# Optimization experiments

Measured on AMD Instinct MI355X. Metric: run time of the kernel, lower is better.

Reference implementation:

```python
import jax, jax.numpy as jnp
import numpy as np
from jax import lax

NSTEPS = 7
BN_EPS = 1e-5


def setup_inputs() -> dict:
    key = jax.random.key(0)
    ks = jax.random.split(key, 7)
    bs, in_ch, h, w, k = 8, 16, 256, 256, 3
    f = jax.random.normal(ks[0], (bs, in_ch, h, w), dtype=jnp.float32)
    vec_w = jax.random.normal(ks[1], (2 * in_ch, in_ch, k, k), dtype=jnp.float32) * 0.1
    vec_b = jax.random.normal(ks[2], (2 * in_ch,), dtype=jnp.float32) * 0.1
    bn_gamma = jnp.ones((2 * in_ch,), dtype=jnp.float32)
    bn_beta = jnp.zeros((2 * in_ch,), dtype=jnp.float32)
    fuse_w = jax.random.normal(ks[3], (in_ch, in_ch, NSTEPS, 1, 1), dtype=jnp.float32) * 0.1
    fuse_b = jax.random.normal(ks[4], (in_ch,), dtype=jnp.float32) * 0.1
    return {"f": f, "vec_w": vec_w, "vec_b": vec_b, "bn_gamma": bn_gamma,
            "bn_beta": bn_beta, "fuse_w": fuse_w, "fuse_b": fuse_b}


def _bilinear_sample(src, py, px):
    """Bilinear sample with zero padding (torch grid_sample align_corners=True).
    src: [N,C,H,W]; py,px: [N,H,W] pixel coordinates (row, col)."""
    N, C, H, W = src.shape
    y0 = jnp.floor(py); x0 = jnp.floor(px)
    wy1 = py - y0; wy0 = 1.0 - wy1
    wx1 = px - x0; wx0 = 1.0 - wx1
    src_flat = src.reshape(N, C, H * W)

    def gather(yi, xi):
        valid = (yi >= 0) & (yi <= H - 1) & (xi >= 0) & (xi <= W - 1)
        yc = jnp.clip(yi, 0, H - 1).astype(jnp.int32)
        xc = jnp.clip(xi, 0, W - 1).astype(jnp.int32)
        idx = (yc * W + xc).reshape(N, 1, H * W)
        vals = jnp.take_along_axis(src_flat, idx, axis=2).reshape(N, C, H, W)
        return vals * valid.astype(src.dtype)[:, None, :, :]

    out = (wy0 * wx0)[:, None] * gather(y0, x0) \
        + (wy0 * wx1)[:, None] * gather(y0, x0 + 1) \
        + (wy1 * wx0)[:, None] * gather(y0 + 1, x0) \
        + (wy1 * wx1)[:, None] * gather(y0 + 1, x0 + 1)
    return out


def _warp(src, flow, grid_y, grid_x):
    # grid + flow in pixel space; original normalizes to [-1,1] then grid_sample
    # un-normalizes with align_corners=True, which is exactly pixel coords grid+flow.
    py = grid_y[None] + flow[:, 0]
    px = grid_x[None] + flow[:, 1]
    return _bilinear_sample(src, py, px)


def reference(f, vec_w, vec_b, bn_gamma, bn_beta, fuse_w, fuse_b):
    bs, in_ch, h, w = f.shape
    # vec_conv + BatchNorm2d (training-mode batch stats, biased variance)
    vec = lax.conv_general_dilated(f, vec_w, (1, 1), [(1, 1), (1, 1)],
                                   dimension_numbers=("NCHW", "OIHW", "NCHW"))
    vec = vec + vec_b[None, :, None, None]
    mean = vec.mean(axis=(0, 2, 3))
    var = vec.var(axis=(0, 2, 3))
    vec = bn_gamma[None, :, None, None] * (vec - mean[None, :, None, None]) \
        * lax.rsqrt(var + BN_EPS)[None, :, None, None] + bn_beta[None, :, None, None]

    c = vec.shape[1]  # = 2*in_ch
    vec = vec.reshape(bs * c // 2, 2, h, w)  # per-channel 2D flow fields

    grid_y, grid_x = jnp.meshgrid(jnp.arange(h, dtype=f.dtype),
                                  jnp.arange(w, dtype=f.dtype), indexing="ij")

    # VecInt: scaling and squaring, keeping every intermediate deformation
    vec = vec * (1.0 / 2 ** NSTEPS)
    deforms = []
    for _ in range(NSTEPS):
        vec = vec + _warp(vec, vec, grid_y, grid_x)
        deforms.append(vec)

    fsrc = f.reshape(bs * in_ch, 1, h, w)
    maps = [_warp(fsrc, d, grid_y, grid_x).reshape(bs, in_ch, h, w) for d in deforms]
    stacked = jnp.stack(maps, axis=2)  # [bs, in_ch, nsteps, h, w]

    # Conv3d with kernel (nsteps,1,1) then squeeze -> per-pixel channel/step mix
    out = jnp.einsum("ocs,bcshw->bohw", fuse_w[:, :, :, 0, 0], stacked)
    out = out + fuse_b[None, :, None, None]
    return out
```

## Files before the change

### kernel.cpp

```cpp
#include <hip/hip_runtime.h>
#include <hip/hip_fp16.h>

#define H 256
#define W 256
#define BS 8
#define IC 16
#define OCH 32
#define NSTEPS 7
#define PLANE (H*W)
#define NFIELDS (BS*IC)
#define BN_N (BS*PLANE)
#define BN_EPS 1e-5f
#define PW 260
#define PSZ (260 * 260)

__global__ void transpose_w_kernel(const float* __restrict__ w,
                                   __half2* __restrict__ wTh) {
    for (int idx = threadIdx.x; idx < IC * 9 * 16; idx += blockDim.x) {
        int rc = idx >> 4;
        int p  = idx & 15;
        float lo = w[(2 * p) * (IC * 9) + rc];
        float hi = w[(2 * p + 1) * (IC * 9) + rc];
        wTh[idx] = __floats2half2_rn(lo, hi);
    }
}

__global__ void guard_zero_kernel(unsigned* __restrict__ bufA,
                                  unsigned* __restrict__ bufB,
                                  unsigned short* __restrict__ f16p) {
    int p = blockIdx.x;
    size_t pb = (size_t)p * PSZ;
    for (int i = threadIdx.x; i < 2064; i += blockDim.x) {
        int row, col;
        if (i < 1040) {
            int r = i / 260;
            row = (r == 0) ? 0 : 256 + r;
            col = i - r * 260;
        } else {
            int j = i - 1040;
            int c = j / 256;
            col = (c == 0) ? 0 : 256 + c;
            row = 1 + (j - c * 256);
        }
        size_t off = pb + (size_t)row * PW + col;
        bufA[off] = 0u;
        bufB[off] = 0u;
        f16p[off] = 0;
    }
}

__global__ __launch_bounds__(256, 4) void conv_kernel(
    const float* __restrict__ f, const __half2* __restrict__ wTh,
    const float* __restrict__ vec_b, __half2* __restrict__ vec_out,
    __half* __restrict__ f16p) {
    __shared__ __align__(16) __half sf[16][18][40];

    int blk = blockIdx.x;
    int xcd = blk & 7;
    int i   = blk >> 3;
    int b   = i >> 4;
    int j   = i & 15;
    int ty0 = ((xcd << 1) | (j >> 3)) * 16;
    int tx0 = (j & 7) * 32;
    int tid = threadIdx.x;
    int tyl = tid >> 5, txl = tid & 31;
    int y0p = ty0 + tyl, y1p = ty0 + tyl + 8, x = tx0 + txl;

    {
        int sic = tid >> 4;
        int st  = tid & 15;
        if (st < 10) {
            int gx0 = tx0 - 4 + 4 * st;
            const float* fpl = f + (size_t)(b * IC + sic) * PLANE;
            size_t fb16 = (size_t)(b * IC + sic) * PSZ;
            bool full = (gx0 >= 0) && (gx0 + 3 < W);
            bool own  = (st >= 1) && (st <= 8);
#pragma unroll
            for (int r = 0; r < 18; ++r) {
                int gy = ty0 - 1 + r;
                float4 v = make_float4(0.f, 0.f, 0.f, 0.f);
                if ((unsigned)gy < (unsigned)H) {
                    if (full) {
                        v = *(const float4*)(fpl + (size_t)gy * W + gx0);
                    } else {
                        if ((unsigned)(gx0 + 0) < (unsigned)W) v.x = fpl[(size_t)gy * W + gx0 + 0];
                        if ((unsigned)(gx0 + 1) < (unsigned)W) v.y = fpl[(size_t)gy * W + gx0 + 1];
                        if ((unsigned)(gx0 + 2) < (unsigned)W) v.z = fpl[(size_t)gy * W + gx0 + 2];
                        if ((unsigned)(gx0 + 3) < (unsigned)W) v.w = fpl[(size_t)gy * W + gx0 + 3];
                    }
                }
                __half2 h01 = __floats2half2_rn(v.x, v.y);
                __half2 h23 = __floats2half2_rn(v.z, v.w);
                union { __half2 h[2]; float2 f2; } u;
                u.h[0] = h01; u.h[1] = h23;
                *(float2*)&sf[sic][r][4 * st] = u.f2;
                if (own && r >= 1 && r <= 16) {
                    __half* fp = f16p + fb16 + (size_t)(gy + 1) * PW + (gx0 + 1);
                    fp[0] = __low2half(h01);
                    fp[1] = __high2half(h01);
                    fp[2] = __low2half(h23);
                    fp[3] = __high2half(h23);
                }
            }
        }
    }

    __half2 acc0[16], acc1[16];
#pragma unroll
    for (int p = 0; p < 16; ++p) {
        __half2 bp = __floats2half2_rn(vec_b[2 * p], vec_b[2 * p + 1]);
        acc0[p] = bp; acc1[p] = bp;
    }

    __syncthreads();

#pragma unroll 2
    for (int ic = 0; ic < 16; ++ic) {
#pragma unroll
        for (int k = 0; k < 9; ++k) {
            int ky = k / 3, kx = k - ky * 3;
            __half2 fv0 = __half2half2(sf[ic][tyl + ky][txl + kx + 3]);
            __half2 fv1 = __half2half2(sf[ic][tyl + 8 + ky][txl + kx + 3]);
            const __half2* wrow = wTh + (ic * 9 + k) * 16;
#pragma unroll
            for (int p = 0; p < 16; ++p) {
                __half2 wv = wrow[p];
                acc0[p] = __hfma2(fv0, wv, acc0[p]);
                acc1[p] = __hfma2(fv1, wv, acc1[p]);
            }
        }
    }

#pragma unroll
    for (int c = 0; c < IC; ++c) {
        size_t pb = (size_t)(b * IC + c) * PLANE;
        vec_out[pb + y0p * W + x] = acc0[c];
        vec_out[pb + y1p * W + x] = acc1[c];
    }
}

__global__ __launch_bounds__(256) void stats_kernel(
    const __half2* __restrict__ vec, float* __restrict__ stats) {
    int blk   = blockIdx.x;
    int n     = blk >> 4;
    int chunk = blk & 15;
    const float4* p4 = (const float4*)(vec + (size_t)n * PLANE + chunk * 4096);
    int tid = threadIdx.x;

    float s0 = 0.f, s1 = 0.f, q0 = 0.f, q1 = 0.f;
#pragma unroll 2
    for (int i = tid; i < 1024; i += 256) {
        float4 w = p4[i];
        const __half2* hh = (const __half2*)&w;
#pragma unroll
        for (int q = 0; q < 4; ++q) {
            float2 v = __half22float2(hh[q]);
            s0 += v.x; s1 += v.y;
            q0 = fmaf(v.x, v.x, q0);
            q1 = fmaf(v.y, v.y, q1);
        }
    }
#pragma unroll
    for (int off = 32; off > 0; off >>= 1) {
        s0 += __shfl_down(s0, off, 64);
        s1 += __shfl_down(s1, off, 64);
        q0 += __shfl_down(q0, off, 64);
        q1 += __shfl_down(q1, off, 64);
    }
    __shared__ float red[4][4];
    int wave = tid >> 6, lane = tid & 63;
    if (lane == 0) {
        red[wave][0] = s0; red[wave][1] = s1;
        red[wave][2] = q0; red[wave][3] = q1;
    }
    __syncthreads();
    if (tid == 0) {
        float t0 = 0.f, t1 = 0.f, t2 = 0.f, t3 = 0.f;
#pragma unroll
        for (int wv = 0; wv < 4; ++wv) {
            t0 += red[wv][0]; t1 += red[wv][1];
            t2 += red[wv][2]; t3 += red[wv][3];
        }
        int ch0 = 2 * (n & 15);
        atomicAdd(stats + ch0,          t0);
        atomicAdd(stats + ch0 + 1,      t1);
        atomicAdd(stats + 32 + ch0,     t2);
        atomicAdd(stats + 32 + ch0 + 1, t3);
    }
}

__global__ void finalize_kernel(const float* __restrict__ stats,
                                const float* __restrict__ gamma,
                                const float* __restrict__ beta,
                                float* __restrict__ AB) {
    int ch = threadIdx.x;
    if (ch < 2 * IC) {
        const float invN = 1.f / (float)BN_N;
        float mean = stats[ch] * invN;
        float var  = stats[32 + ch] * invN - mean * mean;
        float rs   = rsqrtf(var + BN_EPS);
        float a    = gamma[ch] * rs;
        AB[ch]      = a * (1.f / 128.f);
        AB[32 + ch] = (beta[ch] - a * mean) * (1.f / 128.f);
    }
}

__device__ __forceinline__ void tap_setup(float py, float px,
                                          int* o, float* wt) {
    float ffy = floorf(py), ffx = floorf(px);
    int y0 = (int)ffy, x0 = (int)ffx;
    float wy1 = py - ffy, wy0 = 1.f - wy1;
    float wx1 = px - ffx, wx0 = 1.f - wx1;
    bool vy0 = (unsigned)y0 < (unsigned)H, vy1 = (unsigned)(y0 + 1) < (unsigned)H;
    bool vx0 = (unsigned)x0 < (unsigned)W, vx1 = (unsigned)(x0 + 1) < (unsigned)W;
    int yc0 = min(max(y0, 0), H - 1), yc1 = min(max(y0 + 1, 0), H - 1);
    int xc0 = min(max(x0, 0), W - 1), xc1 = min(max(x0 + 1, 0), W - 1);
    o[0] = yc0 * W + xc0; o[1] = yc0 * W + xc1;
    o[2] = yc1 * W + xc0; o[3] = yc1 * W + xc1;
    wt[0] = (vy0 && vx0) ? wy0 * wx0 : 0.f;
    wt[1] = (vy0 && vx1) ? wy0 * wx1 : 0.f;
    wt[2] = (vy1 && vx0) ? wy1 * wx0 : 0.f;
    wt[3] = (vy1 && vx1) ? wy1 * wx1 : 0.f;
}

__device__ __forceinline__ void tap_fast(float py, float px,
                                         int& o, float* wt) {
    float pyc = fminf(fmaxf(py, -1.f), 256.f);
    float pxc = fminf(fmaxf(px, -1.f), 256.f);
    float fy = floorf(pyc), fx = floorf(pxc);
    int y0 = (int)fy, x0 = (int)fx;
    float wy1 = pyc - fy, wy0 = 1.f - wy1;
    float wx1 = pxc - fx, wx0 = 1.f - wx1;
    o = (y0 + 1) * PW + (x0 + 1);
    wt[0] = wy0 * wx0; wt[1] = wy0 * wx1;
    wt[2] = wy1 * wx0; wt[3] = wy1 * wx1;
}

template <bool FIRST, bool LAST>
__global__ __launch_bounds__(256) void step_kernel(
    const __half2* __restrict__ vinRaw, const __half2* __restrict__ vinPad,
    __half2* __restrict__ voutPad, const __half* __restrict__ f16p,
    const float* __restrict__ AB, const float* __restrict__ fw,
    const float* __restrict__ fb, __half* __restrict__ accp,
    float* __restrict__ out, int step) {
    int blk = blockIdx.x;
    int xcd = blk & 7;
    int i   = blk >> 3;
    int b   = i >> 5;
    int h   = (xcd << 5) | (i & 31);
    int tx  = threadIdx.x;
    int idx_raw = h * W + tx;
    int idx_pad = (h + 1) * PW + tx + 1;
    const size_t baseR = (size_t)b * IC * PLANE;
    const size_t baseP = (size_t)b * IC * PSZ;

    float mv[IC];

#pragma unroll 2
    for (int g = 0; g < 4; ++g) {
        float a0j[4], b0j[4], a1j[4], b1j[4];
        float fy[4], fx[4];
        float wt[4][4];
        int   ob[4];
        int   om[4][4];
        const __half2* pl[4];
        float2 vc[4];

#pragma unroll
        for (int j = 0; j < 4; ++j) {
            int c = 4 * g + j;
            if (FIRST) {
                pl[j] = vinRaw + baseR + (size_t)c * PLANE;
                vc[j] = __half22float2(pl[j][idx_raw]);
            } else {
                pl[j] = vinPad + baseP + (size_t)c * PSZ;
                vc[j] = __half22float2(pl[j][idx_pad]);
            }
        }

#pragma unroll
        for (int j = 0; j < 4; ++j) {
            int c = 4 * g + j;
            if (FIRST) {
                a0j[j] = AB[2 * c];     b0j[j] = AB[32 + 2 * c];
                a1j[j] = AB[2 * c + 1]; b1j[j] = AB[32 + 2 * c + 1];
                fy[j] = fmaf(a0j[j], vc[j].x, b0j[j]);
                fx[j] = fmaf(a1j[j], vc[j].y, b1j[j]);
                tap_setup((float)h + fy[j], (float)tx + fx[j], om[j], wt[j]);
            } else {
                fy[j] = vc[j].x;
                fx[j] = vc[j].y;
                tap_fast((float)h + fy[j], (float)tx + fx[j], ob[j], wt[j]);
            }
        }

        float2 t[4][4];
#pragma unroll
        for (int j = 0; j < 4; ++j) {
            if (FIRST) {
#pragma unroll
                for (int k = 0; k < 4; ++k)
                    t[j][k] = __half22float2(pl[j][om[j][k]]);
            } else {
                t[j][0] = __half22float2(pl[j][ob[j]]);
                t[j][1] = __half22float2(pl[j][ob[j] + 1]);
                t[j][2] = __half22float2(pl[j][ob[j] + PW]);
                t[j][3] = __half22float2(pl[j][ob[j] + PW + 1]);
            }
        }

        float ny[4], nx[4];
        int   pb_[4];
        float pw_[4][4];
#pragma unroll
        for (int j = 0; j < 4; ++j) {
            int c = 4 * g + j;
            float Sy = wt[j][0] * t[j][0].x + wt[j][1] * t[j][1].x
                     + wt[j][2] * t[j][2].x + wt[j][3] * t[j][3].x;
            float Sx = wt[j][0] * t[j][0].y + wt[j][1] * t[j][1].y
                     + wt[j][2] * t[j][2].y + wt[j][3] * t[j][3].y;
            if (FIRST) {
                float Ws = wt[j][0] + wt[j][1] + wt[j][2] + wt[j][3];
                ny[j] = fy[j] + fmaf(a0j[j], Sy, b0j[j] * Ws);
                nx[j] = fx[j] + fmaf(a1j[j], Sx, b1j[j] * Ws);
            } else {
                ny[j] = fy[j] + Sy;
                nx[j] = fx[j] + Sx;
            }
            if (!LAST)
                voutPad[baseP + (size_t)c * PSZ + idx_pad] =
                    __float22half2_rn(make_float2(ny[j], nx[j]));
            tap_fast((float)h + ny[j], (float)tx + nx[j], pb_[j], pw_[j]);
        }

#pragma unroll
        for (int j = 0; j < 4; ++j) {
            int c = 4 * g + j;
            const __half* fp = f16p + baseP + (size_t)c * PSZ;
            mv[c] = pw_[j][0] * __half2float(fp[pb_[j]])
                  + pw_[j][1] * __half2float(fp[pb_[j] + 1])
                  + pw_[j][2] * __half2float(fp[pb_[j] + PW])
                  + pw_[j][3] * __half2float(fp[pb_[j] + PW + 1]);
        }
    }

    __half* ap = accp + ((size_t)b * PLANE + idx_raw) * IC;
    float prev[IC];
    if (!FIRST) {
        float4 p0 = ((const float4*)ap)[0];
        float4 p1 = ((const float4*)ap)[1];
        const __half2* ph = (const __half2*)&p0;
#pragma unroll
        for (int k = 0; k < 4; ++k) {
            float2 v = __half22float2(ph[k]);
            prev[2 * k] = v.x; prev[2 * k + 1] = v.y;
        }
        const __half2* qh = (const __half2*)&p1;
#pragma unroll
        for (int k = 0; k < 4; ++k) {
            float2 v = __half22float2(qh[k]);
            prev[8 + 2 * k] = v.x; prev[8 + 2 * k + 1] = v.y;
        }
    }

    float a[IC];
#pragma unroll
    for (int o2 = 0; o2 < IC; ++o2) {
        a[o2] = FIRST ? fb[o2] : prev[o2];
#pragma unroll
        for (int c = 0; c < IC; ++c)
            a[o2] = fmaf(fw[(o2 * IC + c) * NSTEPS + step], mv[c], a[o2]);
    }

    if (LAST) {
#pragma unroll
        for (int o2 = 0; o2 < IC; ++o2)
            out[baseR + (size_t)o2 * PLANE + idx_raw] = a[o2];
    } else {
        float4 s0, s1;
        __half2* sh = (__half2*)&s0;
#pragma unroll
        for (int k = 0; k < 4; ++k)
            sh[k] = __float22half2_rn(make_float2(a[2 * k], a[2 * k + 1]));
        __half2* th = (__half2*)&s1;
#pragma unroll
        for (int k = 0; k < 4; ++k)
            th[k] = __float22half2_rn(make_float2(a[8 + 2 * k], a[9 + 2 * k]));
        ((float4*)ap)[0] = s0;
        ((float4*)ap)[1] = s1;
    }
}

extern "C" void kernel_launch(void* const* d_in, const int* in_sizes, int n_in,
                              void* d_out, int out_size, void* d_ws,
                              size_t ws_size, hipStream_t stream) {
    const float* f      = (const float*)d_in[0];
    const float* vec_w  = (const float*)d_in[1];
    const float* vec_b  = (const float*)d_in[2];
    const float* gamma  = (const float*)d_in[3];
    const float* beta   = (const float*)d_in[4];
    const float* fuse_w = (const float*)d_in[5];
    const float* fuse_b = (const float*)d_in[6];
    float* out = (float*)d_out;

    char* ws = (char*)d_ws;
    const size_t rawB  = (size_t)NFIELDS * PLANE * sizeof(__half2);
    const size_t padB2 = (size_t)NFIELDS * PSZ * sizeof(__half2);
    const size_t padB1 = (size_t)NFIELDS * PSZ * sizeof(__half);
    const size_t accB  = (size_t)NFIELDS * PLANE * sizeof(__half);
    __half2* bufRaw = (__half2*)ws;
    __half2* bufA   = (__half2*)(ws + rawB);
    __half2* bufB   = (__half2*)(ws + rawB + padB2);
    __half*  f16p   = (__half*)(ws + rawB + 2 * padB2);
    __half*  accp   = (__half*)(ws + rawB + 2 * padB2 + padB1);
    __half2* wTh    = (__half2*)(ws + rawB + 2 * padB2 + padB1 + accB);
    float*   stats  = (float*)(wTh + IC * 9 * 16);
    float*   AB     = stats + 64;

    hipMemsetAsync(stats, 0, 64 * sizeof(float), stream);
    transpose_w_kernel<<<1, 512, 0, stream>>>(vec_w, wTh);
    guard_zero_kernel<<<NFIELDS, 256, 0, stream>>>(
        (unsigned*)bufA, (unsigned*)bufB, (unsigned short*)f16p);
    conv_kernel<<<1024, 256, 0, stream>>>(f, wTh, vec_b, bufRaw, f16p);
    stats_kernel<<<NFIELDS * 16, 256, 0, stream>>>(bufRaw, stats);
    finalize_kernel<<<1, 64, 0, stream>>>(stats, gamma, beta, AB);

    for (int s = 0; s < NSTEPS; ++s) {
        const __half2* vinPad = (s & 1) ? bufA : bufB;
        __half2*       voutP  = (s & 1) ? bufB : bufA;
        if (s == 0)
            step_kernel<true, false><<<2048, 256, 0, stream>>>(
                bufRaw, (const __half2*)nullptr, bufA, f16p, AB,
                fuse_w, fuse_b, accp, out, s);
        else if (s < NSTEPS - 1)
            step_kernel<false, false><<<2048, 256, 0, stream>>>(
                (const __half2*)nullptr, vinPad, voutP, f16p, AB,
                fuse_w, fuse_b, accp, out, s);
        else
            step_kernel<false, true><<<2048, 256, 0, stream>>>(
                (const __half2*)nullptr, vinPad, (__half2*)nullptr, f16p, AB,
                fuse_w, fuse_b, accp, out, s);
    }
}
```

Measured before the change: 495.2 us.

## Store source image as horizontally duplicated half2 pairs for bilinear gathers

Adds a dup_kernel that writes each source pixel together with its right neighbour as a half2 into a padded buffer. Each bilinear sample of f in the step kernels then needs two 32-bit loads instead of four 16-bit loads. The conv kernel no longer writes the padded fp16 copy, and its tile shrinks to 8 rows per block with one accumulator set, doubling the grid and raising the launch-bounds occupancy hint. The cost is an extra kernel launch and a padded image buffer twice as large.

After: 510.9 us. 1.03x slower.

```diff
diff --git a/kernel.cpp b/kernel.cpp
--- a/kernel.cpp
+++ b/kernel.cpp
@@ -27,7 +27,7 @@
 
 __global__ void guard_zero_kernel(unsigned* __restrict__ bufA,
                                   unsigned* __restrict__ bufB,
-                                  unsigned short* __restrict__ f16p) {
+                                  unsigned* __restrict__ dup) {
     int p = blockIdx.x;
     size_t pb = (size_t)p * PSZ;
     for (int i = threadIdx.x; i < 2064; i += blockDim.x) {
@@ -45,26 +45,42 @@
         size_t off = pb + (size_t)row * PW + col;
         bufA[off] = 0u;
         bufB[off] = 0u;
-        f16p[off] = 0;
-    }
-}
-
-__global__ __launch_bounds__(256, 4) void conv_kernel(
+        dup[off] = 0u;
+    }
+}
+
+__global__ __launch_bounds__(256) void dup_kernel(const float* __restrict__ f,
+                                                  __half2* __restrict__ dup) {
+    int blk = blockIdx.x;
+    int p  = blk >> 3;
+    int r0 = (blk & 7) * 32;
+    const float* fp = f + (size_t)p * PLANE;
+    __half2* dp = dup + (size_t)p * PSZ;
+    int tx = threadIdx.x;
+#pragma unroll 4
+    for (int ry = 0; ry < 32; ++ry) {
+        int y = r0 + ry;
+        float a = fp[(size_t)y * W + tx];
+        float b = (tx < W - 1) ? fp[(size_t)y * W + tx + 1] : 0.f;
+        dp[(size_t)(y + 1) * PW + tx + 1] = __floats2half2_rn(a, b);
+        if (tx == 0)
+            dp[(size_t)(y + 1) * PW] = __floats2half2_rn(0.f, a);
+    }
+}
+
+__global__ __launch_bounds__(256, 8) void conv_kernel(
     const float* __restrict__ f, const __half2* __restrict__ wTh,
-    const float* __restrict__ vec_b, __half2* __restrict__ vec_out,
-    __half* __restrict__ f16p) {
-    __shared__ __align__(16) __half sf[16][18][40];
+    const float* __restrict__ vec_b, __half2* __restrict__ vec_out) {
+    __shared__ __align__(16) __half sf[16][10][40];
 
     int blk = blockIdx.x;
     int xcd = blk & 7;
     int i   = blk >> 3;
-    int b   = i >> 4;
-    int j   = i & 15;
-    int ty0 = ((xcd << 1) | (j >> 3)) * 16;
+    int b   = i >> 5;
+    int j   = i & 31;
+    int ty0 = ((xcd << 2) | (j >> 3)) * 8;
     int tx0 = (j & 7) * 32;
     int tid = threadIdx.x;
-    int tyl = tid >> 5, txl = tid & 31;
-    int y0p = ty0 + tyl, y1p = ty0 + tyl + 8, x = tx0 + txl;
 
     {
         int sic = tid >> 4;
@@ -72,11 +88,9 @@
         if (st < 10) {
             int gx0 = tx0 - 4 + 4 * st;
             const float* fpl = f + (size_t)(b * IC + sic) * PLANE;
-            size_t fb16 = (size_t)(b * IC + sic) * PSZ;
             bool full = (gx0 >= 0) && (gx0 + 3 < W);
-            bool own  = (st >= 1) && (st <= 8);
-#pragma unroll
-            for (int r = 0; r < 18; ++r) {
+#pragma unroll
+            for (int r = 0; r < 10; ++r) {
                 int gy = ty0 - 1 + r;
                 float4 v = make_float4(0.f, 0.f, 0.f, 0.f);
                 if ((unsigned)gy < (unsigned)H) {
@@ -89,54 +103,39 @@
                         if ((unsigned)(gx0 + 3) < (unsigned)W) v.w = fpl[(size_t)gy * W + gx0 + 3];
                     }
                 }
-                __half2 h01 = __floats2half2_rn(v.x, v.y);
-                __half2 h23 = __floats2half2_rn(v.z, v.w);
                 union { __half2 h[2]; float2 f2; } u;
-                u.h[0] = h01; u.h[1] = h23;
+                u.h[0] = __floats2half2_rn(v.x, v.y);
+                u.h[1] = __floats2half2_rn(v.z, v.w);
                 *(float2*)&sf[sic][r][4 * st] = u.f2;
-                if (own && r >= 1 && r <= 16) {
-                    __half* fp = f16p + fb16 + (size_t)(gy + 1) * PW + (gx0 + 1);
-                    fp[0] = __low2half(h01);
-                    fp[1] = __high2half(h01);
-                    fp[2] = __low2half(h23);
-                    fp[3] = __high2half(h23);
-                }
             }
         }
     }
 
-    __half2 acc0[16], acc1[16];
-#pragma unroll
-    for (int p = 0; p < 16; ++p) {
-        __half2 bp = __floats2half2_rn(vec_b[2 * p], vec_b[2 * p + 1]);
-        acc0[p] = bp; acc1[p] = bp;
-    }
+    __half2 acc[16];
+#pragma unroll
+    for (int p = 0; p < 16; ++p)
+        acc[p] = __floats2half2_rn(vec_b[2 * p], vec_b[2 * p + 1]);
 
     __syncthreads();
 
+    int tyl = tid >> 5, txl = tid & 31;
 #pragma unroll 2
     for (int ic = 0; ic < 16; ++ic) {
 #pragma unroll
         for (int k = 0; k < 9; ++k) {
             int ky = k / 3, kx = k - ky * 3;
-            __half2 fv0 = __half2half2(sf[ic][tyl + ky][txl + kx + 3]);
-            __half2 fv1 = __half2half2(sf[ic][tyl + 8 + ky][txl + kx + 3]);
+            __half2 fv = __half2half2(sf[ic][tyl + ky][txl + kx + 3]);
             const __half2* wrow = wTh + (ic * 9 + k) * 16;
 #pragma unroll
-            for (int p = 0; p < 16; ++p) {
-                __half2 wv = wrow[p];
-                acc0[p] = __hfma2(fv0, wv, acc0[p]);
-                acc1[p] = __hfma2(fv1, wv, acc1[p]);
-            }
-        }
-    }
-
-#pragma unroll
-    for (int c = 0; c < IC; ++c) {
-        size_t pb = (size_t)(b * IC + c) * PLANE;
-        vec_out[pb + y0p * W + x] = acc0[c];
-        vec_out[pb + y1p * W + x] = acc1[c];
-    }
+            for (int p = 0; p < 16; ++p)
+                acc[p] = __hfma2(fv, wrow[p], acc[p]);
+        }
+    }
+
+    int y = ty0 + tyl, x = tx0 + txl;
+#pragma unroll
+    for (int c = 0; c < IC; ++c)
+        vec_out[(size_t)(b * IC + c) * PLANE + (size_t)y * W + x] = acc[c];
 }
 
 __global__ __launch_bounds__(256) void stats_kernel(
@@ -239,7 +238,7 @@
 template <bool FIRST, bool LAST>
 __global__ __launch_bounds__(256) void step_kernel(
     const __half2* __restrict__ vinRaw, const __half2* __restrict__ vinPad,
-    __half2* __restrict__ voutPad, const __half* __restrict__ f16p,
+    __half2* __restrict__ voutPad, const __half2* __restrict__ fdup,
     const float* __restrict__ AB, const float* __restrict__ fw,
     const float* __restrict__ fb, __half* __restrict__ accp,
     float* __restrict__ out, int step) {
@@ -336,11 +335,11 @@
 #pragma unroll
         for (int j = 0; j < 4; ++j) {
             int c = 4 * g + j;
-            const __half* fp = f16p + baseP + (size_t)c * PSZ;
-            mv[c] = pw_[j][0] * __half2float(fp[pb_[j]])
-                  + pw_[j][1] * __half2float(fp[pb_[j] + 1])
-                  + pw_[j][2] * __half2float(fp[pb_[j] + PW])
-                  + pw_[j][3] * __half2float(fp[pb_[j] + PW + 1]);
+            const __half2* fdp = fdup + baseP + (size_t)c * PSZ;
+            float2 g0 = __half22float2(fdp[pb_[j]]);
+            float2 g1 = __half22float2(fdp[pb_[j] + PW]);
+            mv[c] = pw_[j][0] * g0.x + pw_[j][1] * g0.y
+                  + pw_[j][2] * g1.x + pw_[j][3] * g1.y;
         }
     }
 
@@ -406,22 +405,22 @@
     char* ws = (char*)d_ws;
     const size_t rawB  = (size_t)NFIELDS * PLANE * sizeof(__half2);
     const size_t padB2 = (size_t)NFIELDS * PSZ * sizeof(__half2);
-    const size_t padB1 = (size_t)NFIELDS * PSZ * sizeof(__half);
     const size_t accB  = (size_t)NFIELDS * PLANE * sizeof(__half);
     __half2* bufRaw = (__half2*)ws;
     __half2* bufA   = (__half2*)(ws + rawB);
     __half2* bufB   = (__half2*)(ws + rawB + padB2);
-    __half*  f16p   = (__half*)(ws + rawB + 2 * padB2);
-    __half*  accp   = (__half*)(ws + rawB + 2 * padB2 + padB1);
-    __half2* wTh    = (__half2*)(ws + rawB + 2 * padB2 + padB1 + accB);
+    __half2* fdup   = (__half2*)(ws + rawB + 2 * padB2);
+    __half*  accp   = (__half*)(ws + rawB + 3 * padB2);
+    __half2* wTh    = (__half2*)(ws + rawB + 3 * padB2 + accB);
     float*   stats  = (float*)(wTh + IC * 9 * 16);
     float*   AB     = stats + 64;
 
     hipMemsetAsync(stats, 0, 64 * sizeof(float), stream);
     transpose_w_kernel<<<1, 512, 0, stream>>>(vec_w, wTh);
     guard_zero_kernel<<<NFIELDS, 256, 0, stream>>>(
-        (unsigned*)bufA, (unsigned*)bufB, (unsigned short*)f16p);
-    conv_kernel<<<1024, 256, 0, stream>>>(f, wTh, vec_b, bufRaw, f16p);
+        (unsigned*)bufA, (unsigned*)bufB, (unsigned*)fdup);
+    dup_kernel<<<NFIELDS * 8, 256, 0, stream>>>(f, fdup);
+    conv_kernel<<<2048, 256, 0, stream>>>(f, wTh, vec_b, bufRaw);
     stats_kernel<<<NFIELDS * 16, 256, 0, stream>>>(bufRaw, stats);
     finalize_kernel<<<1, 64, 0, stream>>>(stats, gamma, beta, AB);
 
@@ -430,15 +429,15 @@
         __half2*       voutP  = (s & 1) ? bufB : bufA;
         if (s == 0)
             step_kernel<true, false><<<2048, 256, 0, stream>>>(
-                bufRaw, (const __half2*)nullptr, bufA, f16p, AB,
+                bufRaw, (const __half2*)nullptr, bufA, fdup, AB,
                 fuse_w, fuse_b, accp, out, s);
         else if (s < NSTEPS - 1)
             step_kernel<false, false><<<2048, 256, 0, stream>>>(
-                (const __half2*)nullptr, vinPad, voutP, f16p, AB,
+                (const __half2*)nullptr, vinPad, voutP, fdup, AB,
                 fuse_w, fuse_b, accp, out, s);
         else
             step_kernel<false, true><<<2048, 256, 0, stream>>>(
-                (const __half2*)nullptr, vinPad, (__half2*)nullptr, f16p, AB,
+                (const __half2*)nullptr, vinPad, (__half2*)nullptr, fdup, AB,
                 fuse_w, fuse_b, accp, out, s);
     }
 }
```
